# Kernel optimization log

Hardware: AMD Instinct MI355X
Metric: run time of the kernel (lower is better)

## Reference

```python
import jax, jax.numpy as jnp
import numpy as np

B, EH, T = 8, 768, 512
PH, U = 320, 128
JH, C = 320, 34


def setup_inputs() -> dict:
    key = jax.random.key(0)
    ks = jax.random.split(key, 8)
    s_enc = 1.0 / np.sqrt(EH)
    s_pred = 1.0 / np.sqrt(PH)
    s_out = 1.0 / np.sqrt(JH)
    return {
        "enc": jax.random.normal(ks[0], (B, EH, T), dtype=jnp.float32),
        "dec": jax.random.normal(ks[1], (B, PH, U), dtype=jnp.float32),
        "W_enc": jax.random.normal(ks[2], (JH, EH), dtype=jnp.float32) * s_enc,
        "b_enc": jax.random.normal(ks[3], (JH,), dtype=jnp.float32) * s_enc,
        "W_pred": jax.random.normal(ks[4], (JH, PH), dtype=jnp.float32) * s_pred,
        "b_pred": jax.random.normal(ks[5], (JH,), dtype=jnp.float32) * s_pred,
        "W_out": jax.random.normal(ks[6], (C, JH), dtype=jnp.float32) * s_out,
        "b_out": jax.random.normal(ks[7], (C,), dtype=jnp.float32) * s_out,
    }


def reference(enc, dec, W_enc, b_enc, W_pred, b_pred, W_out, b_out):
    # enc: (B, EH, T) channels-first -> project each frame: (B, T, JH)
    e = jnp.einsum("bht,jh->btj", enc, W_enc) + b_enc
    # dec: (B, PH, U) -> (B, U, JH)
    p = jnp.einsum("bhu,ju->buj".replace("u,ju", "u,jh").replace("bhu", "bhu"), dec, W_pred) + b_pred if False else jnp.einsum("bhu,jh->buj", dec, W_pred) + b_pred
    # broadcast sum -> (B, T, U, JH), ReLU, small linear, log_softmax over classes
    h = jax.nn.relu(e[:, :, None, :] + p[:, None, :, :])
    logits = jnp.einsum("btuj,cj->btuc", h, W_out) + b_out
    return jax.nn.log_softmax(logits, axis=-1)
```

## Files before the change

### kernel.cpp

```cpp
#include <hip/hip_runtime.h>

#define B_ 8
#define EH_ 768
#define T_ 512
#define PH_ 320
#define U_ 128
#define JH_ 320
#define C_ 34
#define LDP 328

typedef _Float16 f16x8 __attribute__((ext_vector_type(8)));
typedef _Float16 f16x4 __attribute__((ext_vector_type(4)));
typedef float f32x4 __attribute__((ext_vector_type(4)));

static __device__ __forceinline__ f16x8 relu_sum8(f16x8 a, f16x8 b) {
    f16x8 s = a + b;
    f16x8 z = (f16x8)(_Float16)0.f;
    return __builtin_elementwise_max(s, z);
}

__global__ __launch_bounds__(256) void prep_kernel(
    const float* __restrict__ enc, const float* __restrict__ dec,
    const float* __restrict__ Wenc, const float* __restrict__ Wpred,
    const float* __restrict__ Wout,
    _Float16* __restrict__ enc_t, _Float16* __restrict__ dec_t,
    _Float16* __restrict__ wenc, _Float16* __restrict__ wpred,
    _Float16* __restrict__ wout)
{
    __shared__ _Float16 tile[32][36];
    const int NE = 16 * 24 * B_;
    const int ND = 4 * 10 * B_;
    const int tid = threadIdx.x;
    int bid = blockIdx.x;

    if (bid < NE + ND) {
        const float* src; _Float16* dst; int H, N, n0, h0, b;
        if (bid < NE) {
            src = enc; dst = enc_t; H = EH_; N = T_;
            n0 = (bid % 16) * 32; h0 = ((bid / 16) % 24) * 32; b = bid / (16 * 24);
        } else {
            int i = bid - NE;
            src = dec; dst = dec_t; H = PH_; N = U_;
            n0 = (i % 4) * 32; h0 = ((i / 4) % 10) * 32; b = i / 40;
        }
        const int tx = tid & 7, ty = tid >> 3;
        float4 v = *(const float4*)&src[((size_t)b * H + h0 + ty) * N + n0 + tx * 4];
        f16x4 t;
        t[0] = (_Float16)v.x; t[1] = (_Float16)v.y; t[2] = (_Float16)v.z; t[3] = (_Float16)v.w;
        *(f16x4*)&tile[ty][tx * 4] = t;
        __syncthreads();
        f16x4 o;
        o[0] = tile[tx * 4 + 0][ty];
        o[1] = tile[tx * 4 + 1][ty];
        o[2] = tile[tx * 4 + 2][ty];
        o[3] = tile[tx * 4 + 3][ty];
        *(f16x4*)&dst[((size_t)b * N + n0 + ty) * H + h0 + tx * 4] = o;
    } else {
        const int t1 = JH_ * EH_, t2 = JH_ * PH_, t3 = C_ * JH_;
        int i = (bid - NE - ND) * 256 + tid;
        if (i < t1)                wenc[i] = (_Float16)Wenc[i];
        else if (i < t1 + t2)      wpred[i - t1] = (_Float16)Wpred[i - t1];
        else if (i < t1 + t2 + t3) wout[i - t1 - t2] = (_Float16)Wout[i - t1 - t2];
    }
}

__global__ __launch_bounds__(256) void proj_kernel(
    const _Float16* __restrict__ enc_t, const _Float16* __restrict__ dec_t,
    const _Float16* __restrict__ wenc, const _Float16* __restrict__ wpred,
    const float* __restrict__ b_enc, const float* __restrict__ b_pred,
    _Float16* __restrict__ e_f, _Float16* __restrict__ p_f)
{
    const int tid = threadIdx.x;
    const int wave = tid >> 6, lane = tid & 63;
    const int lrow = lane & 15, quad = lane >> 4;

    int wid = blockIdx.x * 4 + wave;
    const int We = (T_ / 16) * (JH_ / 16) * B_;
    const _Float16 *src, *W; const float* bias; _Float16* dst; int H, N;
    if (wid < We) { src = enc_t; W = wenc;  bias = b_enc;  dst = e_f; H = EH_; N = T_; }
    else { wid -= We; src = dec_t; W = wpred; bias = b_pred; dst = p_f; H = PH_; N = U_; }

    const int ntn = N / 16;
    const int nt = wid % ntn; int r = wid / ntn;
    const int jt = r % (JH_ / 16); const int b = r / (JH_ / 16);
    const int n0 = nt * 16, j0 = jt * 16;

    const _Float16* ap = src + ((size_t)b * N + n0 + lrow) * H + quad * 8;
    const _Float16* wp = W + (size_t)(j0 + lrow) * H + quad * 8;

    f32x4 acc = {0.f, 0.f, 0.f, 0.f};
#pragma unroll 4
    for (int k = 0; k < H; k += 32) {
        f16x8 af = *(const f16x8*)(ap + k);
        f16x8 wf = *(const f16x8*)(wp + k);
        acc = __builtin_amdgcn_mfma_f32_16x16x32_f16(wf, af, acc, 0, 0, 0);
    }
    const float4 bj = *(const float4*)&bias[j0 + quad * 4];
    f16x4 o;
    o[0] = (_Float16)(acc[0] + bj.x);
    o[1] = (_Float16)(acc[1] + bj.y);
    o[2] = (_Float16)(acc[2] + bj.z);
    o[3] = (_Float16)(acc[3] + bj.w);
    *(f16x4*)&dst[((size_t)b * N + n0 + lrow) * JH_ + j0 + quad * 4] = o;
}

__global__ __launch_bounds__(256) void joint_kernel(
    const _Float16* __restrict__ e_f, const _Float16* __restrict__ p_f,
    const _Float16* __restrict__ wout_f, const float* __restrict__ b_out,
    float* __restrict__ out)
{
    __shared__ alignas(16) _Float16 lds[(34 + 32 + 8) * LDP];

    const int tid = threadIdx.x;
    const int t0 = blockIdx.x * 8;
    const int u0 = blockIdx.y * 32;
    const int b  = blockIdx.z;

    {
        const uint4* sw = (const uint4*)wout_f;
        for (int i = tid; i < 34 * 40; i += 256) {
            int rr = i / 40, k8 = i % 40;
            *(uint4*)&lds[rr * LDP + k8 * 8] = sw[i];
        }
        const uint4* sp = (const uint4*)(p_f + ((size_t)b * U_ + u0) * JH_);
        for (int i = tid; i < 32 * 40; i += 256) {
            int rr = i / 40, k8 = i % 40;
            *(uint4*)&lds[(34 + rr) * LDP + k8 * 8] = sp[i];
        }
        const uint4* se = (const uint4*)(e_f + ((size_t)b * T_ + t0) * JH_);
        for (int i = tid; i < 8 * 40; i += 256) {
            int rr = i / 40, k8 = i % 40;
            *(uint4*)&lds[(66 + rr) * LDP + k8 * 8] = se[i];
        }
    }
    __syncthreads();

    const int lane = tid & 63, wave = tid >> 6;
    const int lrow = lane & 15, quad = lane >> 4;
    const int lk = quad * 8;
    const int urow  = 34 + (wave & 1) * 16 + lrow;
    const int tbase = 66 + (wave >> 1) * 4;

    f32x4 acc[4][3];
#pragma unroll
    for (int tt = 0; tt < 4; ++tt)
#pragma unroll
        for (int c = 0; c < 3; ++c) acc[tt][c] = (f32x4){0.f, 0.f, 0.f, 0.f};

    for (int kk = 0; kk < 10; ++kk) {
        const int k = lk + kk * 32;
        f16x8 pv = *(const f16x8*)&lds[urow * LDP + k];
        f16x8 w0 = *(const f16x8*)&lds[(0  + lrow) * LDP + k];
        f16x8 w1 = *(const f16x8*)&lds[(16 + lrow) * LDP + k];
        f16x8 w2 = *(const f16x8*)&lds[(32 + lrow) * LDP + k];
#pragma unroll
        for (int tt = 0; tt < 4; ++tt) {
            f16x8 ev = *(const f16x8*)&lds[(tbase + tt) * LDP + k];
            f16x8 h = relu_sum8(pv, ev);
            acc[tt][0] = __builtin_amdgcn_mfma_f32_16x16x32_f16(w0, h, acc[tt][0], 0, 0, 0);
            acc[tt][1] = __builtin_amdgcn_mfma_f32_16x16x32_f16(w1, h, acc[tt][1], 0, 0, 0);
            acc[tt][2] = __builtin_amdgcn_mfma_f32_16x16x32_f16(w2, h, acc[tt][2], 0, 0, 0);
        }
    }

    const float4 bq0 = *(const float4*)&b_out[quad * 4];
    const float4 bq1 = *(const float4*)&b_out[16 + quad * 4];
    const bool q0 = (quad == 0);
    float b2x = 0.f, b2y = 0.f;
    if (q0) { b2x = b_out[32]; b2y = b_out[33]; }

    const int u = u0 + (wave & 1) * 16 + lrow;
#pragma unroll
    for (int tt = 0; tt < 4; ++tt) {
        float v0[4], v1[4];
        v0[0] = acc[tt][0][0] + bq0.x; v0[1] = acc[tt][0][1] + bq0.y;
        v0[2] = acc[tt][0][2] + bq0.z; v0[3] = acc[tt][0][3] + bq0.w;
        v1[0] = acc[tt][1][0] + bq1.x; v1[1] = acc[tt][1][1] + bq1.y;
        v1[2] = acc[tt][1][2] + bq1.z; v1[3] = acc[tt][1][3] + bq1.w;
        float v2x = q0 ? (acc[tt][2][0] + b2x) : -INFINITY;
        float v2y = q0 ? (acc[tt][2][1] + b2y) : -INFINITY;

        float m = fmaxf(fmaxf(fmaxf(v0[0], v0[1]), fmaxf(v0[2], v0[3])),
                        fmaxf(fmaxf(v1[0], v1[1]), fmaxf(v1[2], v1[3])));
        m = fmaxf(m, fmaxf(v2x, v2y));
        m = fmaxf(m, __shfl_xor(m, 16));
        m = fmaxf(m, __shfl_xor(m, 32));

        float s = __expf(v0[0] - m) + __expf(v0[1] - m) + __expf(v0[2] - m) + __expf(v0[3] - m)
                + __expf(v1[0] - m) + __expf(v1[1] - m) + __expf(v1[2] - m) + __expf(v1[3] - m);
        if (q0) s += __expf(v2x - m) + __expf(v2y - m);
        s += __shfl_xor(s, 16);
        s += __shfl_xor(s, 32);
        const float lse = m + __logf(s);

        const int t = t0 + (wave >> 1) * 4 + tt;
        float* po = out + (((size_t)b * T_ + t) * U_ + u) * C_;
        *(float2*)&po[quad * 4]          = make_float2(v0[0] - lse, v0[1] - lse);
        *(float2*)&po[quad * 4 + 2]      = make_float2(v0[2] - lse, v0[3] - lse);
        *(float2*)&po[16 + quad * 4]     = make_float2(v1[0] - lse, v1[1] - lse);
        *(float2*)&po[16 + quad * 4 + 2] = make_float2(v1[2] - lse, v1[3] - lse);
        if (q0) *(float2*)&po[32]        = make_float2(v2x - lse, v2y - lse);
    }
}

extern "C" void kernel_launch(void* const* d_in, const int* in_sizes, int n_in,
                              void* d_out, int out_size, void* d_ws, size_t ws_size,
                              hipStream_t stream) {
    const float* enc    = (const float*)d_in[0];
    const float* dec    = (const float*)d_in[1];
    const float* W_enc  = (const float*)d_in[2];
    const float* b_enc  = (const float*)d_in[3];
    const float* W_pred = (const float*)d_in[4];
    const float* b_pred = (const float*)d_in[5];
    const float* W_out  = (const float*)d_in[6];
    const float* b_out  = (const float*)d_in[7];
    float* out = (float*)d_out;

    _Float16* enc_t  = (_Float16*)d_ws;
    _Float16* dec_t  = enc_t  + (size_t)B_ * T_ * EH_;
    _Float16* wenc_f = dec_t  + (size_t)B_ * U_ * PH_;
    _Float16* wpred_f= wenc_f + (size_t)JH_ * EH_;
    _Float16* wout_f = wpred_f+ (size_t)JH_ * PH_;
    _Float16* e_f    = wout_f + (size_t)C_ * JH_;
    _Float16* p_f    = e_f    + (size_t)B_ * T_ * JH_;

    const int NE = 16 * 24 * B_, ND = 4 * 10 * B_;
    const int NW = (JH_ * EH_ + JH_ * PH_ + C_ * JH_ + 255) / 256;
    prep_kernel<<<dim3(NE + ND + NW), 256, 0, stream>>>(
        enc, dec, W_enc, W_pred, W_out, enc_t, dec_t, wenc_f, wpred_f, wout_f);

    const int We = (T_ / 16) * (JH_ / 16) * B_;
    const int Wp = (U_ / 16) * (JH_ / 16) * B_;
    proj_kernel<<<dim3((We + Wp) / 4), 256, 0, stream>>>(
        enc_t, dec_t, wenc_f, wpred_f, b_enc, b_pred, e_f, p_f);

    joint_kernel<<<dim3(T_ / 8, U_ / 32, B_), 256, 0, stream>>>(e_f, p_f, wout_f, b_out, out);
}
```

Baseline: 153.0 us.

## Register-block projection GEMM 2x2 and read zero-padded W_out from global

The projection kernel now gives each wave a 32x32 output tile built from four MFMA accumulators, so every loaded A and W fragment is used twice and fewer waves are launched. The joint kernel stops staging W_out in LDS. It reads a copy zero-padded to 48 rows straight from global memory (cache-resident), which shrinks the LDS footprint and drops the staging loop. It also adds an occupancy hint of 4 blocks per SM. The trade-offs are more global/L1 traffic for W_out inside the inner loop and fewer, larger waves in the projection.

```diff
diff --git a/kernel.cpp b/kernel.cpp
--- a/kernel.cpp
+++ b/kernel.cpp
@@ -25,7 +25,7 @@
     const float* __restrict__ Wout,
     _Float16* __restrict__ enc_t, _Float16* __restrict__ dec_t,
     _Float16* __restrict__ wenc, _Float16* __restrict__ wpred,
-    _Float16* __restrict__ wout)
+    _Float16* __restrict__ wout48)
 {
     __shared__ _Float16 tile[32][36];
     const int NE = 16 * 24 * B_;
@@ -56,11 +56,15 @@
         o[3] = tile[tx * 4 + 3][ty];
         *(f16x4*)&dst[((size_t)b * N + n0 + ty) * H + h0 + tx * 4] = o;
     } else {
-        const int t1 = JH_ * EH_, t2 = JH_ * PH_, t3 = C_ * JH_;
+        const int t1 = JH_ * EH_, t2 = JH_ * PH_, t3 = 48 * JH_;
         int i = (bid - NE - ND) * 256 + tid;
         if (i < t1)                wenc[i] = (_Float16)Wenc[i];
         else if (i < t1 + t2)      wpred[i - t1] = (_Float16)Wpred[i - t1];
-        else if (i < t1 + t2 + t3) wout[i - t1 - t2] = (_Float16)Wout[i - t1 - t2];
+        else if (i < t1 + t2 + t3) {
+            int k = i - t1 - t2;
+            int c = k / JH_;
+            wout48[k] = (c < C_) ? (_Float16)Wout[k] : (_Float16)0.f;
+        }
     }
 }
 
@@ -75,41 +79,58 @@
     const int lrow = lane & 15, quad = lane >> 4;
 
     int wid = blockIdx.x * 4 + wave;
-    const int We = (T_ / 16) * (JH_ / 16) * B_;
-    const _Float16 *src, *W; const float* bias; _Float16* dst; int H, N;
-    if (wid < We) { src = enc_t; W = wenc;  bias = b_enc;  dst = e_f; H = EH_; N = T_; }
-    else { wid -= We; src = dec_t; W = wpred; bias = b_pred; dst = p_f; H = PH_; N = U_; }
-
-    const int ntn = N / 16;
+    const int We = (T_ / 32) * (JH_ / 32) * B_;
+    const _Float16 *src, *W; const float* bias; _Float16* dst; int H, N, ntn;
+    if (wid < We) { src = enc_t; W = wenc;  bias = b_enc;  dst = e_f; H = EH_; N = T_; ntn = T_ / 32; }
+    else { wid -= We; src = dec_t; W = wpred; bias = b_pred; dst = p_f; H = PH_; N = U_; ntn = U_ / 32; }
+
     const int nt = wid % ntn; int r = wid / ntn;
-    const int jt = r % (JH_ / 16); const int b = r / (JH_ / 16);
-    const int n0 = nt * 16, j0 = jt * 16;
-
-    const _Float16* ap = src + ((size_t)b * N + n0 + lrow) * H + quad * 8;
-    const _Float16* wp = W + (size_t)(j0 + lrow) * H + quad * 8;
-
-    f32x4 acc = {0.f, 0.f, 0.f, 0.f};
-#pragma unroll 4
+    const int jt = r % (JH_ / 32); const int b = r / (JH_ / 32);
+    const int n0 = nt * 32, j0 = jt * 32;
+
+    const _Float16* a0p = src + ((size_t)b * N + n0 + lrow) * H + quad * 8;
+    const _Float16* a1p = a0p + (size_t)16 * H;
+    const _Float16* w0p = W + (size_t)(j0 + lrow) * H + quad * 8;
+    const _Float16* w1p = w0p + (size_t)16 * H;
+
+    f32x4 acc00 = {0.f,0.f,0.f,0.f}, acc01 = {0.f,0.f,0.f,0.f};
+    f32x4 acc10 = {0.f,0.f,0.f,0.f}, acc11 = {0.f,0.f,0.f,0.f};
+
+#pragma unroll 2
     for (int k = 0; k < H; k += 32) {
-        f16x8 af = *(const f16x8*)(ap + k);
-        f16x8 wf = *(const f16x8*)(wp + k);
-        acc = __builtin_amdgcn_mfma_f32_16x16x32_f16(wf, af, acc, 0, 0, 0);
-    }
-    const float4 bj = *(const float4*)&bias[j0 + quad * 4];
-    f16x4 o;
-    o[0] = (_Float16)(acc[0] + bj.x);
-    o[1] = (_Float16)(acc[1] + bj.y);
-    o[2] = (_Float16)(acc[2] + bj.z);
-    o[3] = (_Float16)(acc[3] + bj.w);
-    *(f16x4*)&dst[((size_t)b * N + n0 + lrow) * JH_ + j0 + quad * 4] = o;
-}
-
-__global__ __launch_bounds__(256) void joint_kernel(
+        f16x8 a0 = *(const f16x8*)(a0p + k);
+        f16x8 a1 = *(const f16x8*)(a1p + k);
+        f16x8 w0 = *(const f16x8*)(w0p + k);
+        f16x8 w1 = *(const f16x8*)(w1p + k);
+        acc00 = __builtin_amdgcn_mfma_f32_16x16x32_f16(w0, a0, acc00, 0, 0, 0);
+        acc01 = __builtin_amdgcn_mfma_f32_16x16x32_f16(w0, a1, acc01, 0, 0, 0);
+        acc10 = __builtin_amdgcn_mfma_f32_16x16x32_f16(w1, a0, acc10, 0, 0, 0);
+        acc11 = __builtin_amdgcn_mfma_f32_16x16x32_f16(w1, a1, acc11, 0, 0, 0);
+    }
+
+#pragma unroll
+    for (int jt2 = 0; jt2 < 2; ++jt2) {
+        const float4 bj = *(const float4*)&bias[j0 + jt2 * 16 + quad * 4];
+#pragma unroll
+        for (int nt2 = 0; nt2 < 2; ++nt2) {
+            const f32x4 ac = jt2 ? (nt2 ? acc11 : acc10) : (nt2 ? acc01 : acc00);
+            f16x4 o;
+            o[0] = (_Float16)(ac[0] + bj.x);
+            o[1] = (_Float16)(ac[1] + bj.y);
+            o[2] = (_Float16)(ac[2] + bj.z);
+            o[3] = (_Float16)(ac[3] + bj.w);
+            const int n = n0 + nt2 * 16 + lrow;
+            *(f16x4*)&dst[((size_t)b * N + n) * JH_ + j0 + jt2 * 16 + quad * 4] = o;
+        }
+    }
+}
+
+__global__ __launch_bounds__(256, 4) void joint_kernel(
     const _Float16* __restrict__ e_f, const _Float16* __restrict__ p_f,
-    const _Float16* __restrict__ wout_f, const float* __restrict__ b_out,
+    const _Float16* __restrict__ wout48, const float* __restrict__ b_out,
     float* __restrict__ out)
 {
-    __shared__ alignas(16) _Float16 lds[(34 + 32 + 8) * LDP];
+    __shared__ alignas(16) _Float16 lds[40 * LDP];
 
     const int tid = threadIdx.x;
     const int t0 = blockIdx.x * 8;
@@ -117,20 +138,15 @@
     const int b  = blockIdx.z;
 
     {
-        const uint4* sw = (const uint4*)wout_f;
-        for (int i = tid; i < 34 * 40; i += 256) {
-            int rr = i / 40, k8 = i % 40;
-            *(uint4*)&lds[rr * LDP + k8 * 8] = sw[i];
-        }
         const uint4* sp = (const uint4*)(p_f + ((size_t)b * U_ + u0) * JH_);
         for (int i = tid; i < 32 * 40; i += 256) {
             int rr = i / 40, k8 = i % 40;
-            *(uint4*)&lds[(34 + rr) * LDP + k8 * 8] = sp[i];
+            *(uint4*)&lds[rr * LDP + k8 * 8] = sp[i];
         }
         const uint4* se = (const uint4*)(e_f + ((size_t)b * T_ + t0) * JH_);
         for (int i = tid; i < 8 * 40; i += 256) {
             int rr = i / 40, k8 = i % 40;
-            *(uint4*)&lds[(66 + rr) * LDP + k8 * 8] = se[i];
+            *(uint4*)&lds[(32 + rr) * LDP + k8 * 8] = se[i];
         }
     }
     __syncthreads();
@@ -138,8 +154,12 @@
     const int lane = tid & 63, wave = tid >> 6;
     const int lrow = lane & 15, quad = lane >> 4;
     const int lk = quad * 8;
-    const int urow  = 34 + (wave & 1) * 16 + lrow;
-    const int tbase = 66 + (wave >> 1) * 4;
+    const int urow  = (wave & 1) * 16 + lrow;
+    const int tbase = 32 + (wave >> 1) * 4;
+
+    const _Float16* w0p = wout48 + (size_t)lrow * JH_ + lk;
+    const _Float16* w1p = w0p + (size_t)16 * JH_;
+    const _Float16* w2p = w0p + (size_t)32 * JH_;
 
     f32x4 acc[4][3];
 #pragma unroll
@@ -147,15 +167,16 @@
 #pragma unroll
         for (int c = 0; c < 3; ++c) acc[tt][c] = (f32x4){0.f, 0.f, 0.f, 0.f};
 
+#pragma unroll 2
     for (int kk = 0; kk < 10; ++kk) {
-        const int k = lk + kk * 32;
-        f16x8 pv = *(const f16x8*)&lds[urow * LDP + k];
-        f16x8 w0 = *(const f16x8*)&lds[(0  + lrow) * LDP + k];
-        f16x8 w1 = *(const f16x8*)&lds[(16 + lrow) * LDP + k];
-        f16x8 w2 = *(const f16x8*)&lds[(32 + lrow) * LDP + k];
+        const int k = kk * 32;
+        f16x8 w0 = *(const f16x8*)(w0p + k);
+        f16x8 w1 = *(const f16x8*)(w1p + k);
+        f16x8 w2 = *(const f16x8*)(w2p + k);
+        f16x8 pv = *(const f16x8*)&lds[urow * LDP + lk + k];
 #pragma unroll
         for (int tt = 0; tt < 4; ++tt) {
-            f16x8 ev = *(const f16x8*)&lds[(tbase + tt) * LDP + k];
+            f16x8 ev = *(const f16x8*)&lds[(tbase + tt) * LDP + lk + k];
             f16x8 h = relu_sum8(pv, ev);
             acc[tt][0] = __builtin_amdgcn_mfma_f32_16x16x32_f16(w0, h, acc[tt][0], 0, 0, 0);
             acc[tt][1] = __builtin_amdgcn_mfma_f32_16x16x32_f16(w1, h, acc[tt][1], 0, 0, 0);
@@ -221,16 +242,16 @@
     _Float16* wenc_f = dec_t  + (size_t)B_ * U_ * PH_;
     _Float16* wpred_f= wenc_f + (size_t)JH_ * EH_;
     _Float16* wout_f = wpred_f+ (size_t)JH_ * PH_;
-    _Float16* e_f    = wout_f + (size_t)C_ * JH_;
+    _Float16* e_f    = wout_f + (size_t)48 * JH_;
     _Float16* p_f    = e_f    + (size_t)B_ * T_ * JH_;
 
     const int NE = 16 * 24 * B_, ND = 4 * 10 * B_;
-    const int NW = (JH_ * EH_ + JH_ * PH_ + C_ * JH_ + 255) / 256;
+    const int NW = (JH_ * EH_ + JH_ * PH_ + 48 * JH_ + 255) / 256;
     prep_kernel<<<dim3(NE + ND + NW), 256, 0, stream>>>(
         enc, dec, W_enc, W_pred, W_out, enc_t, dec_t, wenc_f, wpred_f, wout_f);
 
-    const int We = (T_ / 16) * (JH_ / 16) * B_;
-    const int Wp = (U_ / 16) * (JH_ / 16) * B_;
+    const int We = (T_ / 32) * (JH_ / 32) * B_;
+    const int Wp = (U_ / 32) * (JH_ / 32) * B_;
     proj_kernel<<<dim3((We + Wp) / 4), 256, 0, stream>>>(
         enc_t, dec_t, wenc_f, wpred_f, b_enc, b_pred, e_f, p_f);
 
```

Result: slower. 160.6 us (+4.9%).
